# Optimization experiments

Hardware: AMD Instinct MI355X
Metric: run time of the kernel (lower is better)

## Reference

```python
import jax, jax.numpy as jnp
import numpy as np

B, N, ADIM, VDIM = 16, 8192, 256, 128
KERN = 4  # edges_to_nodes conv kernel, padding=KERN//2 -> length E -> E+1 = N


def setup_inputs() -> dict:
    key = jax.random.key(0)
    ks = jax.random.split(key, 12)
    pos_0 = jax.random.normal(ks[0], (B, N, 3), dtype=jnp.float32)
    pos_1 = jax.random.normal(ks[1], (B, N, 3), dtype=jnp.float32)
    # VecLinear(4, vdim): W (vdim, 4), init std = fan_in**-0.5
    W_v = jax.random.normal(ks[2], (VDIM, 4), dtype=jnp.float32) * (4 ** -0.5)
    # scalar MLP: Linear(4, adim) -> LeakyReLU(0.2) -> Linear(adim, adim)
    W1 = jax.random.normal(ks[3], (ADIM, 4), dtype=jnp.float32) * (4 ** -0.5)
    b1 = jax.random.normal(ks[4], (ADIM,), dtype=jnp.float32) * 0.02
    W2 = jax.random.normal(ks[5], (ADIM, ADIM), dtype=jnp.float32) * (ADIM ** -0.5)
    b2 = jax.random.normal(ks[6], (ADIM,), dtype=jnp.float32) * 0.02
    # ScalConv1d(adim, 4, edges_to_nodes=True): Conv1d(adim, adim, 4, padding=2), with bias
    K_a = jax.random.normal(ks[7], (ADIM, ADIM, KERN), dtype=jnp.float32) * ((ADIM * KERN) ** -0.5)
    b_a = jax.random.normal(ks[8], (ADIM,), dtype=jnp.float32) * 0.02
    # VecConv1d(vdim, 4, edges_to_nodes=True): Conv1d(vdim, vdim, 4, padding=2), no bias
    K_v = jax.random.normal(ks[9], (VDIM, VDIM, KERN), dtype=jnp.float32) * ((VDIM * KERN) ** -0.5)
    return {"pos_0": pos_0, "pos_1": pos_1, "W_v": W_v, "W1": W1, "b1": b1,
            "W2": W2, "b2": b2, "K_a": K_a, "b_a": b_a, "K_v": K_v}


def _forward(pos_0, pos_1, W_v, W1, b1, W2, b2, K_a, b_a, K_v):
    batch = pos_0.shape[0]
    # relative displacement features on path edges: (B, E, 4, 3), E = N-1
    vecs = jnp.stack([
        pos_0[:, 1:] - pos_0[:, :-1],
        pos_1[:, 1:] - pos_1[:, :-1],
        pos_1[:, :-1] - pos_0[:, 1:],
        pos_1[:, 1:] - pos_0[:, :-1],
    ], axis=2)
    norms = jnp.sqrt(jnp.sum(vecs * vecs, axis=-1))  # (B, E, 4)
    # scalar MLP with LeakyReLU(0.2)
    h = jnp.einsum('bef,af->bea', norms, W1) + b1
    h = jnp.where(h >= 0, h, 0.2 * h)
    y_a = jnp.einsum('bea,oa->beo', h, W2) + b2          # (B, E, adim)
    # VecLinear: 'oi,...ik->...ok'
    y_v = jnp.einsum('oi,beik->beok', W_v, vecs)          # (B, E, vdim, 3)
    dn = ('NCH', 'OIH', 'NCH')
    # ScalConv1d edges_to_nodes: Conv1d(adim, adim, 4, padding=2) -> length E+1 = N
    xa = jnp.transpose(y_a, (0, 2, 1))                    # (B, adim, E)
    a = jax.lax.conv_general_dilated(xa, K_a, (1,), [(2, 2)], dimension_numbers=dn)
    a = a + b_a[None, :, None]
    a_out = jnp.transpose(a, (0, 2, 1))                   # (B, N, adim)
    # VecConv1d edges_to_nodes: fold 3 spatial components into batch, no bias
    xv = jnp.transpose(y_v, (0, 3, 2, 1)).reshape(3 * batch, VDIM, -1)  # (3B, vdim, E)
    v = jax.lax.conv_general_dilated(xv, K_v, (1,), [(2, 2)], dimension_numbers=dn)
    v_out = jnp.transpose(v.reshape(batch, 3, VDIM, -1), (0, 3, 2, 1))  # (B, N, vdim, 3)
    return a_out, v_out


def reference(pos_0, pos_1, W_v, W1, b1, W2, b2, K_a, b_a, K_v):
    return _forward(pos_0, pos_1, W_v, W1, b1, W2, b2, K_a, b_a, K_v)
```

## Files before the change

### kernel.cpp

```cpp
#include <hip/hip_runtime.h>
#include <stdint.h>

#define NN 8192
#define EE 8191
#define AD 256
#define BB 16

typedef unsigned short u16;
typedef short bf16x8 __attribute__((ext_vector_type(8)));
typedef float f32x4 __attribute__((ext_vector_type(4)));
typedef u16 u16x8 __attribute__((ext_vector_type(8)));

__device__ __forceinline__ u16 f2bf(float f) {
  unsigned u = __builtin_bit_cast(unsigned, f);
  u = u + 0x7fffu + ((u >> 16) & 1u);
  return (u16)(u >> 16);
}

__global__ __launch_bounds__(256) void prep_ma(const float* __restrict__ W2,
                                               const float* __restrict__ b2,
                                               const float* __restrict__ K_a,
                                               const float* __restrict__ b_a,
                                               const float* __restrict__ W_v,
                                               const float* __restrict__ K_v,
                                               u16* __restrict__ Ma,
                                               float* __restrict__ bk,
                                               float* __restrict__ bias_all,
                                               float* __restrict__ Mw) {
  __shared__ float ka[256][4];
  __shared__ float b2s[256];
  __shared__ float red[4];
  const int tid = threadIdx.x;
  const int o = blockIdx.x;
  const float4 kv = ((const float4*)K_a)[(size_t)o * 256 + tid];
  ka[tid][0] = kv.x; ka[tid][1] = kv.y; ka[tid][2] = kv.z; ka[tid][3] = kv.w;
  b2s[tid] = b2[tid];
  __syncthreads();
  float acc[4] = {0.f, 0.f, 0.f, 0.f};
  for (int c = 0; c < 256; ++c) {
    const float w = W2[(c << 8) + tid];
    acc[0] += ka[c][0] * w; acc[1] += ka[c][1] * w;
    acc[2] += ka[c][2] * w; acc[3] += ka[c][3] * w;
  }
  const int ac = tid >> 6, ks = (tid >> 5) & 1, jj = tid & 31;
#pragma unroll
  for (int t = 0; t < 4; ++t)
    Ma[((size_t)((t * 8 + ac * 2 + ks) * 256 + o)) * 32 + jj] = f2bf(acc[t]);
  if (tid < 4) {
    float s = 0.f;
    for (int c = 0; c < 256; ++c) s += ka[c][tid] * b2s[c];
    bk[tid * 256 + o] = s;
    red[tid] = s;
  }
  __syncthreads();
  if (tid == 0) bias_all[o] = b_a[o] + red[0] + red[1] + red[2] + red[3];
  if (blockIdx.x == 0) {
    for (int pair = tid; pair < 512; pair += 256) {
      const int k = pair >> 7, ov = pair & 127;
      float c0 = 0.f, c1 = 0.f, c2 = 0.f, c3 = 0.f;
      for (int c = 0; c < 128; ++c) {
        const float kvv = K_v[(size_t)((ov << 7) + c) * 4 + k];
        const float4 wv = ((const float4*)W_v)[c];
        c0 += kvv * wv.x; c1 += kvv * wv.y; c2 += kvv * wv.z; c3 += kvv * wv.w;
      }
      float4 w;
      w.x = -(c0 + c3);
      w.y = c0 - c2;
      w.z = c2 - c1;
      w.w = c1 + c3;
      ((float4*)Mw)[pair] = w;
    }
  }
}

#define MM(Bf, Af, C) __builtin_amdgcn_mfma_f32_16x16x32_bf16((Bf), (Af), (C), 0, 0, 0)

__global__ __launch_bounds__(512, 2) void gemm_fused(const float* __restrict__ p0,
                                                     const float* __restrict__ p1,
                                                     const float* __restrict__ W1,
                                                     const float* __restrict__ b1,
                                                     const u16* __restrict__ Ma,
                                                     const float* __restrict__ bias_all,
                                                     const float* __restrict__ bk,
                                                     const float* __restrict__ Mw,
                                                     float* __restrict__ out) {
  __shared__ __align__(16) char hs[259 * 528];
  __shared__ float nrm[259][4];
  const int tid = threadIdx.x;
  const int lane = tid & 63;
  const int wid = tid >> 6;
  const int wm = wid >> 2, wn = wid & 3;
  const int b = blockIdx.x >> 5;
  const int n0 = (blockIdx.x & 31) * 256;
  const int lhi = lane >> 4;
  const int llo = lane & 15;

  const size_t pbase = (size_t)b * NN * 3;
  for (int idx = tid; idx < 1036; idx += 512) {
    const int rr = idx >> 2, i = idx & 3;
    const int e = n0 + rr - 2;
    float v = 0.f;
    if (e >= 0 && e < EE) {
      const float* P0 = p0 + pbase;
      const float* P1 = p1 + pbase;
      const float* hi = (i == 0) ? P0 + (size_t)(e + 1) * 3
                      : (i == 1) ? P1 + (size_t)(e + 1) * 3
                      : (i == 2) ? P1 + (size_t)e * 3
                                 : P1 + (size_t)(e + 1) * 3;
      const float* lo = (i == 0) ? P0 + (size_t)e * 3
                      : (i == 1) ? P1 + (size_t)e * 3
                      : (i == 2) ? P0 + (size_t)(e + 1) * 3
                                 : P0 + (size_t)e * 3;
      const float dx = hi[0] - lo[0], dy = hi[1] - lo[1], dz = hi[2] - lo[2];
      v = sqrtf(dx * dx + dy * dy + dz * dz);
    }
    nrm[rr][i] = v;
  }
  __syncthreads();

  {
    const int g8 = tid & 31;
    const int strip = tid >> 5;
    float w1r[8][4], b1r[8];
    const float4* W14 = (const float4*)W1;
#pragma unroll
    for (int j = 0; j < 8; ++j) {
      const float4 w = W14[g8 * 8 + j];
      w1r[j][0] = w.x; w1r[j][1] = w.y; w1r[j][2] = w.z; w1r[j][3] = w.w;
      b1r[j] = b1[g8 * 8 + j];
    }
    for (int rr = strip; rr < 259; rr += 16) {
      const int e = n0 + rr - 2;
      const bool valid = (e >= 0) && (e < EE);
      const float nA = nrm[rr][0], nB = nrm[rr][1], nC = nrm[rr][2], nD = nrm[rr][3];
      u16x8 pack;
#pragma unroll
      for (int j = 0; j < 8; ++j) {
        float v = b1r[j] + nA * w1r[j][0] + nB * w1r[j][1] +
                  nC * w1r[j][2] + nD * w1r[j][3];
        v = (v >= 0.f) ? v : 0.2f * v;
        pack[j] = valid ? f2bf(v) : (u16)0;
      }
      const int cs = (g8 & 24) | ((g8 + rr) & 7);
      *(u16x8*)(hs + rr * 528 + (cs << 4)) = pack;
    }
  }
  __syncthreads();

  {
    const int o = tid & 127, ng = tid >> 7;
    const int nstart = n0 + ng * 64;
    const float4* Mw4 = (const float4*)Mw;
    const float4 w0 = Mw4[o], w1 = Mw4[128 + o],
                 w2 = Mw4[256 + o], w3 = Mw4[384 + o];
    float* vb = out + 33554432ULL + (((size_t)b * NN + nstart) * 128 + o) * 3;
    const float* P0 = p0 + pbase;
    const float* P1 = p1 + pbase;
#pragma unroll 1
    for (int jc = 0; jc < 16; ++jc) {
      const int nb = nstart + jc * 4;
      float Ra[8][3], Rp[8][3];
#pragma unroll
      for (int r = 0; r < 8; ++r) {
        int row = nb - 2 + r;
        row = row < 0 ? 0 : (row > NN - 1 ? NN - 1 : row);
        const float* a = P0 + (size_t)row * 3;
        const float* p = P1 + (size_t)row * 3;
        Ra[r][0] = a[0]; Ra[r][1] = a[1]; Ra[r][2] = a[2];
        Rp[r][0] = p[0]; Rp[r][1] = p[1]; Rp[r][2] = p[2];
      }
#pragma unroll
      for (int jj = 0; jj < 4; ++jj) {
        const int n = nb + jj;
        float r0 = 0.f, r1 = 0.f, r2 = 0.f;
#pragma unroll
        for (int k = 0; k < 4; ++k) {
          if (n + k >= 2 && n + k <= NN) {
            const float4 w = (k == 0) ? w0 : (k == 1) ? w1 : (k == 2) ? w2 : w3;
            r0 += w.x * Ra[jj + k][0] + w.y * Ra[jj + k + 1][0] +
                  w.z * Rp[jj + k][0] + w.w * Rp[jj + k + 1][0];
            r1 += w.x * Ra[jj + k][1] + w.y * Ra[jj + k + 1][1] +
                  w.z * Rp[jj + k][1] + w.w * Rp[jj + k + 1][1];
            r2 += w.x * Ra[jj + k][2] + w.y * Ra[jj + k + 1][2] +
                  w.z * Rp[jj + k][2] + w.w * Rp[jj + k + 1][2];
          }
        }
        float* dst = vb + (size_t)(jc * 4 + jj) * 384;
        dst[0] = r0; dst[1] = r1; dst[2] = r2;
      }
    }
  }

  const f32x4 zero = {0.f, 0.f, 0.f, 0.f};
  f32x4 acc[8][4];
#pragma unroll
  for (int m = 0; m < 8; ++m)
#pragma unroll
    for (int nf = 0; nf < 4; ++nf) acc[m][nf] = zero;

  const char* mb = (const char*)Ma + (size_t)(wn * 64 + llo) * 64 + (size_t)lhi * 16;
  const int rb = wm * 128 + llo;
  const int lt = llo + lhi;

  bf16x8 pA0, pA1, pA2, pA3, pB0, pB1, pB2, pB3;
  pA0 = *(const bf16x8*)(mb);
  pA1 = *(const bf16x8*)(mb + 1024);
  pA2 = *(const bf16x8*)(mb + 2048);
  pA3 = *(const bf16x8*)(mb + 3072);

  bf16x8 afA0, afA1, afA2, afA3, afB0, afB1, afB2, afB3;
  {
    const char* ap = hs + rb * 528 + (((lt) & 7) << 4);
    afA0 = *(const bf16x8*)(ap);
    afA1 = *(const bf16x8*)(ap + 8448);
    afA2 = *(const bf16x8*)(ap + 16896);
    afA3 = *(const bf16x8*)(ap + 25344);
  }

#pragma unroll 1
  for (int s = 0; s < 32; s += 2) {
    const int tap = s >> 3;
    const int q = (s >> 1) & 3;
    const int swe = (lt + tap) & 7;
    const char* rowp = hs + (rb + tap) * 528 + (q << 7);
    const char* ape = rowp + (swe << 4);
    const char* apo = rowp + ((swe ^ 4) << 4);
    {
      const char* bp = mb + (size_t)(s + 1) * 16384;
      pB0 = *(const bf16x8*)(bp);
      pB1 = *(const bf16x8*)(bp + 1024);
      pB2 = *(const bf16x8*)(bp + 2048);
      pB3 = *(const bf16x8*)(bp + 3072);
      afB0 = *(const bf16x8*)(ape + 33792);
      afB1 = *(const bf16x8*)(ape + 42240);
      afB2 = *(const bf16x8*)(ape + 50688);
      afB3 = *(const bf16x8*)(ape + 59136);
      acc[0][0] = MM(pA0, afA0, acc[0][0]); acc[1][0] = MM(pA0, afA1, acc[1][0]);
      acc[2][0] = MM(pA0, afA2, acc[2][0]); acc[3][0] = MM(pA0, afA3, acc[3][0]);
      acc[0][1] = MM(pA1, afA0, acc[0][1]); acc[1][1] = MM(pA1, afA1, acc[1][1]);
      acc[2][1] = MM(pA1, afA2, acc[2][1]); acc[3][1] = MM(pA1, afA3, acc[3][1]);
      acc[0][2] = MM(pA2, afA0, acc[0][2]); acc[1][2] = MM(pA2, afA1, acc[1][2]);
      acc[2][2] = MM(pA2, afA2, acc[2][2]); acc[3][2] = MM(pA2, afA3, acc[3][2]);
      acc[0][3] = MM(pA3, afA0, acc[0][3]); acc[1][3] = MM(pA3, afA1, acc[1][3]);
      acc[2][3] = MM(pA3, afA2, acc[2][3]); acc[3][3] = MM(pA3, afA3, acc[3][3]);
      afA0 = *(const bf16x8*)(apo);
      afA1 = *(const bf16x8*)(apo + 8448);
      afA2 = *(const bf16x8*)(apo + 16896);
      afA3 = *(const bf16x8*)(apo + 25344);
      acc[4][0] = MM(pA0, afB0, acc[4][0]); acc[5][0] = MM(pA0, afB1, acc[5][0]);
      acc[6][0] = MM(pA0, afB2, acc[6][0]); acc[7][0] = MM(pA0, afB3, acc[7][0]);
      acc[4][1] = MM(pA1, afB0, acc[4][1]); acc[5][1] = MM(pA1, afB1, acc[5][1]);
      acc[6][1] = MM(pA1, afB2, acc[6][1]); acc[7][1] = MM(pA1, afB3, acc[7][1]);
      acc[4][2] = MM(pA2, afB0, acc[4][2]); acc[5][2] = MM(pA2, afB1, acc[5][2]);
      acc[6][2] = MM(pA2, afB2, acc[6][2]); acc[7][2] = MM(pA2, afB3, acc[7][2]);
      acc[4][3] = MM(pA3, afB0, acc[4][3]); acc[5][3] = MM(pA3, afB1, acc[5][3]);
      acc[6][3] = MM(pA3, afB2, acc[6][3]); acc[7][3] = MM(pA3, afB3, acc[7][3]);
    }
    {
      const int s2 = (s + 2) & 31;
      const char* bp = mb + (size_t)s2 * 16384;
      pA0 = *(const bf16x8*)(bp);
      pA1 = *(const bf16x8*)(bp + 1024);
      pA2 = *(const bf16x8*)(bp + 2048);
      pA3 = *(const bf16x8*)(bp + 3072);
      afB0 = *(const bf16x8*)(apo + 33792);
      afB1 = *(const bf16x8*)(apo + 42240);
      afB2 = *(const bf16x8*)(apo + 50688);
      afB3 = *(const bf16x8*)(apo + 59136);
      acc[0][0] = MM(pB0, afA0, acc[0][0]); acc[1][0] = MM(pB0, afA1, acc[1][0]);
      acc[2][0] = MM(pB0, afA2, acc[2][0]); acc[3][0] = MM(pB0, afA3, acc[3][0]);
      acc[0][1] = MM(pB1, afA0, acc[0][1]); acc[1][1] = MM(pB1, afA1, acc[1][1]);
      acc[2][1] = MM(pB1, afA2, acc[2][1]); acc[3][1] = MM(pB1, afA3, acc[3][1]);
      acc[0][2] = MM(pB2, afA0, acc[0][2]); acc[1][2] = MM(pB2, afA1, acc[1][2]);
      acc[2][2] = MM(pB2, afA2, acc[2][2]); acc[3][2] = MM(pB2, afA3, acc[3][2]);
      acc[0][3] = MM(pB3, afA0, acc[0][3]); acc[1][3] = MM(pB3, afA1, acc[1][3]);
      acc[2][3] = MM(pB3, afA2, acc[2][3]); acc[3][3] = MM(pB3, afA3, acc[3][3]);
      {
        const int tap2 = s2 >> 3;
        const int q2 = (s2 >> 1) & 3;
        const char* ap2 = hs + (rb + tap2) * 528 + (q2 << 7) +
                          ((((lt + tap2) & 7)) << 4);
        afA0 = *(const bf16x8*)(ap2);
        afA1 = *(const bf16x8*)(ap2 + 8448);
        afA2 = *(const bf16x8*)(ap2 + 16896);
        afA3 = *(const bf16x8*)(ap2 + 25344);
      }
      acc[4][0] = MM(pB0, afB0, acc[4][0]); acc[5][0] = MM(pB0, afB1, acc[5][0]);
      acc[6][0] = MM(pB0, afB2, acc[6][0]); acc[7][0] = MM(pB0, afB3, acc[7][0]);
      acc[4][1] = MM(pB1, afB0, acc[4][1]); acc[5][1] = MM(pB1, afB1, acc[5][1]);
      acc[6][1] = MM(pB1, afB2, acc[6][1]); acc[7][1] = MM(pB1, afB3, acc[7][1]);
      acc[4][2] = MM(pB2, afB0, acc[4][2]); acc[5][2] = MM(pB2, afB1, acc[5][2]);
      acc[6][2] = MM(pB2, afB2, acc[6][2]); acc[7][2] = MM(pB2, afB3, acc[7][2]);
      acc[4][3] = MM(pB3, afB0, acc[4][3]); acc[5][3] = MM(pB3, afB1, acc[5][3]);
      acc[6][3] = MM(pB3, afB2, acc[6][3]); acc[7][3] = MM(pB3, afB3, acc[7][3]);
    }
  }

#pragma unroll
  for (int m = 0; m < 8; ++m) {
    const int node = n0 + wm * 128 + m * 16 + llo;
    float* orow = out + ((size_t)b * NN + node) * AD;
    const bool edge = (node <= 1) | (node >= NN - 2);
#pragma unroll
    for (int nf = 0; nf < 4; ++nf) {
      const int o0 = wn * 64 + nf * 16 + lhi * 4;
      float bx = bias_all[o0], by = bias_all[o0 + 1],
            bz = bias_all[o0 + 2], bw = bias_all[o0 + 3];
      if (edge) {
        const float* k0 = bk + o0;
        const float* k1 = bk + 256 + o0;
        const float* k2 = bk + 512 + o0;
        const float* k3 = bk + 768 + o0;
        if (node == 0) {
          bx -= k0[0] + k1[0]; by -= k0[1] + k1[1];
          bz -= k0[2] + k1[2]; bw -= k0[3] + k1[3];
        } else if (node == 1) {
          bx -= k0[0]; by -= k0[1]; bz -= k0[2]; bw -= k0[3];
        } else if (node == NN - 2) {
          bx -= k3[0]; by -= k3[1]; bz -= k3[2]; bw -= k3[3];
        } else {
          bx -= k2[0] + k3[0]; by -= k2[1] + k3[1];
          bz -= k2[2] + k3[2]; bw -= k2[3] + k3[3];
        }
      }
      float4 st;
      st.x = acc[m][nf][0] + bx;
      st.y = acc[m][nf][1] + by;
      st.z = acc[m][nf][2] + bz;
      st.w = acc[m][nf][3] + bw;
      *(float4*)(orow + o0) = st;
    }
  }
}

extern "C" void kernel_launch(void* const* d_in, const int* in_sizes, int n_in,
                              void* d_out, int out_size, void* d_ws, size_t ws_size,
                              hipStream_t stream) {
  const float* pos_0 = (const float*)d_in[0];
  const float* pos_1 = (const float*)d_in[1];
  const float* W_v = (const float*)d_in[2];
  const float* W1 = (const float*)d_in[3];
  const float* b1 = (const float*)d_in[4];
  const float* W2 = (const float*)d_in[5];
  const float* b2 = (const float*)d_in[6];
  const float* K_a = (const float*)d_in[7];
  const float* b_a = (const float*)d_in[8];
  const float* K_v = (const float*)d_in[9];
  float* out = (float*)d_out;
  char* ws = (char*)d_ws;

  const size_t MA_BYTES = (size_t)32 * 256 * 32 * 2;
  u16* Ma = (u16*)(ws);
  float* bk = (float*)(ws + MA_BYTES);
  float* bias_all = (float*)(ws + MA_BYTES + 4096);
  float* Mw = (float*)(ws + MA_BYTES + 4096 + 1024);

  prep_ma<<<dim3(256), dim3(256), 0, stream>>>(W2, b2, K_a, b_a, W_v, K_v,
                                               Ma, bk, bias_all, Mw);
  gemm_fused<<<dim3(512), dim3(512), 0, stream>>>(pos_0, pos_1, W1, b1, Ma,
                                                  bias_all, bk, Mw, out);
}
```

Baseline: 182.7 us.

## Double block to 1024 threads with smaller per-wave MFMA tile and sliding window

The fused kernel now launches 1024-thread blocks (16 waves), and each wave computes a 64-row by 64-column output tile instead of 128 by 64. This halves the accumulator registers, and the A-fragment double-buffer prefetch is dropped in favour of direct LDS loads before each MFMA group. The intent is to put more waves on each CU to hide memory and LDS latency. The vector-conv section now gives each thread 32 nodes and keeps a sliding register window of positions, so it loads only four new rows per step instead of eight. The trade-off is that each wave issues more global loads of the Ma weight fragments relative to its compute, and the A-fragment loads are no longer overlapped with MFMAs.

```diff
diff --git a/kernel.cpp b/kernel.cpp
--- a/kernel.cpp
+++ b/kernel.cpp
@@ -75,15 +75,15 @@
 
 #define MM(Bf, Af, C) __builtin_amdgcn_mfma_f32_16x16x32_bf16((Bf), (Af), (C), 0, 0, 0)
 
-__global__ __launch_bounds__(512, 2) void gemm_fused(const float* __restrict__ p0,
-                                                     const float* __restrict__ p1,
-                                                     const float* __restrict__ W1,
-                                                     const float* __restrict__ b1,
-                                                     const u16* __restrict__ Ma,
-                                                     const float* __restrict__ bias_all,
-                                                     const float* __restrict__ bk,
-                                                     const float* __restrict__ Mw,
-                                                     float* __restrict__ out) {
+__global__ __launch_bounds__(1024, 4) void gemm_fused(const float* __restrict__ p0,
+                                                      const float* __restrict__ p1,
+                                                      const float* __restrict__ W1,
+                                                      const float* __restrict__ b1,
+                                                      const u16* __restrict__ Ma,
+                                                      const float* __restrict__ bias_all,
+                                                      const float* __restrict__ bk,
+                                                      const float* __restrict__ Mw,
+                                                      float* __restrict__ out) {
   __shared__ __align__(16) char hs[259 * 528];
   __shared__ float nrm[259][4];
   const int tid = threadIdx.x;
@@ -96,7 +96,7 @@
   const int llo = lane & 15;
 
   const size_t pbase = (size_t)b * NN * 3;
-  for (int idx = tid; idx < 1036; idx += 512) {
+  for (int idx = tid; idx < 1036; idx += 1024) {
     const int rr = idx >> 2, i = idx & 3;
     const int e = n0 + rr - 2;
     float v = 0.f;
@@ -129,7 +129,7 @@
       w1r[j][0] = w.x; w1r[j][1] = w.y; w1r[j][2] = w.z; w1r[j][3] = w.w;
       b1r[j] = b1[g8 * 8 + j];
     }
-    for (int rr = strip; rr < 259; rr += 16) {
+    for (int rr = strip; rr < 259; rr += 32) {
       const int e = n0 + rr - 2;
       const bool valid = (e >= 0) && (e < EE);
       const float nA = nrm[rr][0], nB = nrm[rr][1], nC = nrm[rr][2], nD = nrm[rr][3];
@@ -149,26 +149,26 @@
 
   {
     const int o = tid & 127, ng = tid >> 7;
-    const int nstart = n0 + ng * 64;
+    const int nstart = n0 + ng * 32;
     const float4* Mw4 = (const float4*)Mw;
     const float4 w0 = Mw4[o], w1 = Mw4[128 + o],
                  w2 = Mw4[256 + o], w3 = Mw4[384 + o];
     float* vb = out + 33554432ULL + (((size_t)b * NN + nstart) * 128 + o) * 3;
     const float* P0 = p0 + pbase;
     const float* P1 = p1 + pbase;
+    float Ra[8][3], Rp[8][3];
+#pragma unroll
+    for (int r = 0; r < 8; ++r) {
+      int row = nstart - 2 + r;
+      row = row < 0 ? 0 : (row > NN - 1 ? NN - 1 : row);
+      const float* a = P0 + (size_t)row * 3;
+      const float* p = P1 + (size_t)row * 3;
+      Ra[r][0] = a[0]; Ra[r][1] = a[1]; Ra[r][2] = a[2];
+      Rp[r][0] = p[0]; Rp[r][1] = p[1]; Rp[r][2] = p[2];
+    }
 #pragma unroll 1
-    for (int jc = 0; jc < 16; ++jc) {
+    for (int jc = 0; jc < 8; ++jc) {
       const int nb = nstart + jc * 4;
-      float Ra[8][3], Rp[8][3];
-#pragma unroll
-      for (int r = 0; r < 8; ++r) {
-        int row = nb - 2 + r;
-        row = row < 0 ? 0 : (row > NN - 1 ? NN - 1 : row);
-        const float* a = P0 + (size_t)row * 3;
-        const float* p = P1 + (size_t)row * 3;
-        Ra[r][0] = a[0]; Ra[r][1] = a[1]; Ra[r][2] = a[2];
-        Rp[r][0] = p[0]; Rp[r][1] = p[1]; Rp[r][2] = p[2];
-      }
 #pragma unroll
       for (int jj = 0; jj < 4; ++jj) {
         const int n = nb + jj;
@@ -188,18 +188,34 @@
         float* dst = vb + (size_t)(jc * 4 + jj) * 384;
         dst[0] = r0; dst[1] = r1; dst[2] = r2;
       }
+      if (jc < 7) {
+#pragma unroll
+        for (int r = 0; r < 4; ++r) {
+          Ra[r][0] = Ra[r + 4][0]; Ra[r][1] = Ra[r + 4][1]; Ra[r][2] = Ra[r + 4][2];
+          Rp[r][0] = Rp[r + 4][0]; Rp[r][1] = Rp[r + 4][1]; Rp[r][2] = Rp[r + 4][2];
+        }
+#pragma unroll
+        for (int r = 4; r < 8; ++r) {
+          int row = nb + 2 + r;
+          row = row > NN - 1 ? NN - 1 : row;
+          const float* a = P0 + (size_t)row * 3;
+          const float* p = P1 + (size_t)row * 3;
+          Ra[r][0] = a[0]; Ra[r][1] = a[1]; Ra[r][2] = a[2];
+          Rp[r][0] = p[0]; Rp[r][1] = p[1]; Rp[r][2] = p[2];
+        }
+      }
     }
   }
 
   const f32x4 zero = {0.f, 0.f, 0.f, 0.f};
-  f32x4 acc[8][4];
-#pragma unroll
-  for (int m = 0; m < 8; ++m)
+  f32x4 acc[4][4];
+#pragma unroll
+  for (int m = 0; m < 4; ++m)
 #pragma unroll
     for (int nf = 0; nf < 4; ++nf) acc[m][nf] = zero;
 
   const char* mb = (const char*)Ma + (size_t)(wn * 64 + llo) * 64 + (size_t)lhi * 16;
-  const int rb = wm * 128 + llo;
+  const int rb = wm * 64 + llo;
   const int lt = llo + lhi;
 
   bf16x8 pA0, pA1, pA2, pA3, pB0, pB1, pB2, pB3;
@@ -207,15 +223,6 @@
   pA1 = *(const bf16x8*)(mb + 1024);
   pA2 = *(const bf16x8*)(mb + 2048);
   pA3 = *(const bf16x8*)(mb + 3072);
-
-  bf16x8 afA0, afA1, afA2, afA3, afB0, afB1, afB2, afB3;
-  {
-    const char* ap = hs + rb * 528 + (((lt) & 7) << 4);
-    afA0 = *(const bf16x8*)(ap);
-    afA1 = *(const bf16x8*)(ap + 8448);
-    afA2 = *(const bf16x8*)(ap + 16896);
-    afA3 = *(const bf16x8*)(ap + 25344);
-  }
 
 #pragma unroll 1
   for (int s = 0; s < 32; s += 2) {
@@ -231,74 +238,44 @@
       pB1 = *(const bf16x8*)(bp + 1024);
       pB2 = *(const bf16x8*)(bp + 2048);
       pB3 = *(const bf16x8*)(bp + 3072);
-      afB0 = *(const bf16x8*)(ape + 33792);
-      afB1 = *(const bf16x8*)(ape + 42240);
-      afB2 = *(const bf16x8*)(ape + 50688);
-      afB3 = *(const bf16x8*)(ape + 59136);
-      acc[0][0] = MM(pA0, afA0, acc[0][0]); acc[1][0] = MM(pA0, afA1, acc[1][0]);
-      acc[2][0] = MM(pA0, afA2, acc[2][0]); acc[3][0] = MM(pA0, afA3, acc[3][0]);
-      acc[0][1] = MM(pA1, afA0, acc[0][1]); acc[1][1] = MM(pA1, afA1, acc[1][1]);
-      acc[2][1] = MM(pA1, afA2, acc[2][1]); acc[3][1] = MM(pA1, afA3, acc[3][1]);
-      acc[0][2] = MM(pA2, afA0, acc[0][2]); acc[1][2] = MM(pA2, afA1, acc[1][2]);
-      acc[2][2] = MM(pA2, afA2, acc[2][2]); acc[3][2] = MM(pA2, afA3, acc[3][2]);
-      acc[0][3] = MM(pA3, afA0, acc[0][3]); acc[1][3] = MM(pA3, afA1, acc[1][3]);
-      acc[2][3] = MM(pA3, afA2, acc[2][3]); acc[3][3] = MM(pA3, afA3, acc[3][3]);
-      afA0 = *(const bf16x8*)(apo);
-      afA1 = *(const bf16x8*)(apo + 8448);
-      afA2 = *(const bf16x8*)(apo + 16896);
-      afA3 = *(const bf16x8*)(apo + 25344);
-      acc[4][0] = MM(pA0, afB0, acc[4][0]); acc[5][0] = MM(pA0, afB1, acc[5][0]);
-      acc[6][0] = MM(pA0, afB2, acc[6][0]); acc[7][0] = MM(pA0, afB3, acc[7][0]);
-      acc[4][1] = MM(pA1, afB0, acc[4][1]); acc[5][1] = MM(pA1, afB1, acc[5][1]);
-      acc[6][1] = MM(pA1, afB2, acc[6][1]); acc[7][1] = MM(pA1, afB3, acc[7][1]);
-      acc[4][2] = MM(pA2, afB0, acc[4][2]); acc[5][2] = MM(pA2, afB1, acc[5][2]);
-      acc[6][2] = MM(pA2, afB2, acc[6][2]); acc[7][2] = MM(pA2, afB3, acc[7][2]);
-      acc[4][3] = MM(pA3, afB0, acc[4][3]); acc[5][3] = MM(pA3, afB1, acc[5][3]);
-      acc[6][3] = MM(pA3, afB2, acc[6][3]); acc[7][3] = MM(pA3, afB3, acc[7][3]);
+      bf16x8 af0 = *(const bf16x8*)(ape);
+      bf16x8 af1 = *(const bf16x8*)(ape + 8448);
+      bf16x8 af2 = *(const bf16x8*)(ape + 16896);
+      bf16x8 af3 = *(const bf16x8*)(ape + 25344);
+      acc[0][0] = MM(pA0, af0, acc[0][0]); acc[1][0] = MM(pA0, af1, acc[1][0]);
+      acc[2][0] = MM(pA0, af2, acc[2][0]); acc[3][0] = MM(pA0, af3, acc[3][0]);
+      acc[0][1] = MM(pA1, af0, acc[0][1]); acc[1][1] = MM(pA1, af1, acc[1][1]);
+      acc[2][1] = MM(pA1, af2, acc[2][1]); acc[3][1] = MM(pA1, af3, acc[3][1]);
+      acc[0][2] = MM(pA2, af0, acc[0][2]); acc[1][2] = MM(pA2, af1, acc[1][2]);
+      acc[2][2] = MM(pA2, af2, acc[2][2]); acc[3][2] = MM(pA2, af3, acc[3][2]);
+      acc[0][3] = MM(pA3, af0, acc[0][3]); acc[1][3] = MM(pA3, af1, acc[1][3]);
+      acc[2][3] = MM(pA3, af2, acc[2][3]); acc[3][3] = MM(pA3, af3, acc[3][3]);
     }
     {
-      const int s2 = (s + 2) & 31;
-      const char* bp = mb + (size_t)s2 * 16384;
+      const int sp = (s + 2 < 32) ? (s + 2) : 31;
+      const char* bp = mb + (size_t)sp * 16384;
       pA0 = *(const bf16x8*)(bp);
       pA1 = *(const bf16x8*)(bp + 1024);
       pA2 = *(const bf16x8*)(bp + 2048);
       pA3 = *(const bf16x8*)(bp + 3072);
-      afB0 = *(const bf16x8*)(apo + 33792);
-      afB1 = *(const bf16x8*)(apo + 42240);
-      afB2 = *(const bf16x8*)(apo + 50688);
-      afB3 = *(const bf16x8*)(apo + 59136);
-      acc[0][0] = MM(pB0, afA0, acc[0][0]); acc[1][0] = MM(pB0, afA1, acc[1][0]);
-      acc[2][0] = MM(pB0, afA2, acc[2][0]); acc[3][0] = MM(pB0, afA3, acc[3][0]);
-      acc[0][1] = MM(pB1, afA0, acc[0][1]); acc[1][1] = MM(pB1, afA1, acc[1][1]);
-      acc[2][1] = MM(pB1, afA2, acc[2][1]); acc[3][1] = MM(pB1, afA3, acc[3][1]);
-      acc[0][2] = MM(pB2, afA0, acc[0][2]); acc[1][2] = MM(pB2, afA1, acc[1][2]);
-      acc[2][2] = MM(pB2, afA2, acc[2][2]); acc[3][2] = MM(pB2, afA3, acc[3][2]);
-      acc[0][3] = MM(pB3, afA0, acc[0][3]); acc[1][3] = MM(pB3, afA1, acc[1][3]);
-      acc[2][3] = MM(pB3, afA2, acc[2][3]); acc[3][3] = MM(pB3, afA3, acc[3][3]);
-      {
-        const int tap2 = s2 >> 3;
-        const int q2 = (s2 >> 1) & 3;
-        const char* ap2 = hs + (rb + tap2) * 528 + (q2 << 7) +
-                          ((((lt + tap2) & 7)) << 4);
-        afA0 = *(const bf16x8*)(ap2);
-        afA1 = *(const bf16x8*)(ap2 + 8448);
-        afA2 = *(const bf16x8*)(ap2 + 16896);
-        afA3 = *(const bf16x8*)(ap2 + 25344);
-      }
-      acc[4][0] = MM(pB0, afB0, acc[4][0]); acc[5][0] = MM(pB0, afB1, acc[5][0]);
-      acc[6][0] = MM(pB0, afB2, acc[6][0]); acc[7][0] = MM(pB0, afB3, acc[7][0]);
-      acc[4][1] = MM(pB1, afB0, acc[4][1]); acc[5][1] = MM(pB1, afB1, acc[5][1]);
-      acc[6][1] = MM(pB1, afB2, acc[6][1]); acc[7][1] = MM(pB1, afB3, acc[7][1]);
-      acc[4][2] = MM(pB2, afB0, acc[4][2]); acc[5][2] = MM(pB2, afB1, acc[5][2]);
-      acc[6][2] = MM(pB2, afB2, acc[6][2]); acc[7][2] = MM(pB2, afB3, acc[7][2]);
-      acc[4][3] = MM(pB3, afB0, acc[4][3]); acc[5][3] = MM(pB3, afB1, acc[5][3]);
-      acc[6][3] = MM(pB3, afB2, acc[6][3]); acc[7][3] = MM(pB3, afB3, acc[7][3]);
-    }
-  }
-
-#pragma unroll
-  for (int m = 0; m < 8; ++m) {
-    const int node = n0 + wm * 128 + m * 16 + llo;
+      bf16x8 af0 = *(const bf16x8*)(apo);
+      bf16x8 af1 = *(const bf16x8*)(apo + 8448);
+      bf16x8 af2 = *(const bf16x8*)(apo + 16896);
+      bf16x8 af3 = *(const bf16x8*)(apo + 25344);
+      acc[0][0] = MM(pB0, af0, acc[0][0]); acc[1][0] = MM(pB0, af1, acc[1][0]);
+      acc[2][0] = MM(pB0, af2, acc[2][0]); acc[3][0] = MM(pB0, af3, acc[3][0]);
+      acc[0][1] = MM(pB1, af0, acc[0][1]); acc[1][1] = MM(pB1, af1, acc[1][1]);
+      acc[2][1] = MM(pB1, af2, acc[2][1]); acc[3][1] = MM(pB1, af3, acc[3][1]);
+      acc[0][2] = MM(pB2, af0, acc[0][2]); acc[1][2] = MM(pB2, af1, acc[1][2]);
+      acc[2][2] = MM(pB2, af2, acc[2][2]); acc[3][2] = MM(pB2, af3, acc[3][2]);
+      acc[0][3] = MM(pB3, af0, acc[0][3]); acc[1][3] = MM(pB3, af1, acc[1][3]);
+      acc[2][3] = MM(pB3, af2, acc[2][3]); acc[3][3] = MM(pB3, af3, acc[3][3]);
+    }
+  }
+
+#pragma unroll
+  for (int m = 0; m < 4; ++m) {
+    const int node = n0 + wm * 64 + m * 16 + llo;
     float* orow = out + ((size_t)b * NN + node) * AD;
     const bool edge = (node <= 1) | (node >= NN - 2);
 #pragma unroll
@@ -357,6 +334,6 @@
 
   prep_ma<<<dim3(256), dim3(256), 0, stream>>>(W2, b2, K_a, b_a, W_v, K_v,
                                                Ma, bk, bias_all, Mw);
-  gemm_fused<<<dim3(512), dim3(512), 0, stream>>>(pos_0, pos_1, W1, b1, Ma,
-                                                  bias_all, bk, Mw, out);
+  gemm_fused<<<dim3(512), dim3(1024), 0, stream>>>(pos_0, pos_1, W1, b1, Ma,
+                                                   bias_all, bk, Mw, out);
 }
```

After: 256.5 us. 1.4x slower.
